# Performance work log

Hardware: AMD Instinct MI355X
Metric: run time of the kernel (lower is better)

## Reference

```python
import jax, jax.numpy as jnp
import numpy as np

B, S, D, H = 2, 2048, 64, 12  # batch, seq, richness (per-head dim), heads
NEG = -99999.0


def setup_inputs() -> dict:
    key = jax.random.key(0)
    ks = jax.random.split(key, 9)
    s_in = 1.0 / np.sqrt(D)
    s_out = 1.0 / np.sqrt(H * D)
    return {
        "x": jax.random.normal(ks[0], (B, S, D), dtype=jnp.float32),
        "Wq": jax.random.uniform(ks[1], (D, H * D), jnp.float32, -s_in, s_in),
        "bq": jax.random.uniform(ks[2], (H * D,), jnp.float32, -s_in, s_in),
        "Wk": jax.random.uniform(ks[3], (D, H * D), jnp.float32, -s_in, s_in),
        "bk": jax.random.uniform(ks[4], (H * D,), jnp.float32, -s_in, s_in),
        "Wv": jax.random.uniform(ks[5], (D, H * D), jnp.float32, -s_in, s_in),
        "bv": jax.random.uniform(ks[6], (H * D,), jnp.float32, -s_in, s_in),
        "Wo": jax.random.uniform(ks[7], (H * D, D), jnp.float32, -s_out, s_out),
        "bo": jax.random.uniform(ks[8], (D,), jnp.float32, -s_out, s_out),
    }


def reference(x, Wq, bq, Wk, bk, Wv, bv, Wo, bo):
    b, s, d = x.shape
    def split_heads(y):
        return y.reshape(b, s, H, d).transpose(0, 2, 1, 3)  # [B,H,S,D]
    q = split_heads(x @ Wq + bq)
    k = split_heads(x @ Wk + bk)
    v = split_heads(x @ Wv + bv)
    # NOTE: no 1/sqrt(d) scaling, faithful to original module.
    scores = jnp.einsum("bhqd,bhkd->bhqk", q, k)  # [B,H,S,S]
    # Faithful quirky mask: tril of the scores, then mask where it's zero.
    mask = jnp.tril(scores)
    scores = jnp.where(mask == 0, NEG, scores)
    p = jax.nn.softmax(scores, axis=-1)
    o = jnp.einsum("bhqk,bhkd->bhqd", p, v)  # [B,H,S,D]
    o = o.transpose(0, 2, 1, 3).reshape(b, s, H * d)
    return o @ Wo + bo
```

## Files before the change

### kernel.cpp

```cpp
#include <hip/hip_runtime.h>
#include <math.h>
#include <type_traits>

#define BB 2
#define SS 2048
#define DD 64
#define HH 12
#define C2FIX 23.083120654223414f

typedef _Float16 v8h __attribute__((ext_vector_type(8)));
typedef short    v8s __attribute__((ext_vector_type(8)));
typedef float    v4f __attribute__((ext_vector_type(4)));
typedef unsigned int v2u __attribute__((ext_vector_type(2)));

__device__ __forceinline__ unsigned short f2bf(float f) {
    unsigned u = __float_as_uint(f);
    u += 0x7FFF + ((u >> 16) & 1);
    return (unsigned short)(u >> 16);
}

__device__ __forceinline__ void async16(const void* g, void* l) {
    __builtin_amdgcn_global_load_lds(
        (const __attribute__((address_space(1))) unsigned int*)g,
        (__attribute__((address_space(3))) unsigned int*)l, 16, 0, 0);
}

__global__ __launch_bounds__(256) void prep_kernel(
    const float* __restrict__ x,
    const float* __restrict__ Wq, const float* __restrict__ Wk,
    const float* __restrict__ Wv, const float* __restrict__ Wo,
    _Float16* __restrict__ x16, _Float16* __restrict__ W16,
    _Float16* __restrict__ WoT)
{
    const int idx = blockIdx.x * 256 + threadIdx.x;
    if (idx < 262144) {
        x16[idx] = (_Float16)x[idx];
    } else if (idx < 262144 + 147456) {
        const int t = idx - 262144;
        const int k = t / 2304, c = t % 2304;
        const int mat = c / 768, cc = c % 768;
        const float* W = (mat == 0) ? Wq : (mat == 1) ? Wk : Wv;
        W16[c * 64 + k] = (_Float16)W[k * 768 + cc];
    } else {
        const int e = idx - 262144 - 147456;
        WoT[(e & 63) * 768 + (e >> 6)] = (_Float16)Wo[e];
    }
}

__global__ __launch_bounds__(256) void qkv_kernel(
    const _Float16* __restrict__ x16, const _Float16* __restrict__ W16,
    const float* __restrict__ bq, const float* __restrict__ bk,
    const float* __restrict__ bv,
    _Float16* __restrict__ Q16, _Float16* __restrict__ K16,
    unsigned short* __restrict__ VT)
{
    const int r0  = blockIdx.x * 64;
    const int c0g = blockIdx.y * 64;
    const int mat = c0g / 768, cc0 = c0g % 768;
    const int h   = cc0 >> 6;
    const int b   = r0 >> 11, s0 = r0 & 2047;

    const int wave = threadIdx.x >> 6, lane = threadIdx.x & 63;
    const int llow = lane & 15, quad = lane >> 4;
    const int rowbase = r0 + 16 * wave;

    const float* bias = (mat == 0) ? bq : (mat == 1) ? bk : bv;

    v8h a0 = *(const v8h*)(x16 + (size_t)(rowbase + llow) * 64 + quad * 8);
    v8h a1 = *(const v8h*)(x16 + (size_t)(rowbase + llow) * 64 + 32 + quad * 8);

    v4f acc[4];
    float bv4[4];
#pragma unroll
    for (int nb = 0; nb < 4; nb++) {
        const int col = c0g + 16 * nb + llow;
        v8h b0 = *(const v8h*)(W16 + (size_t)col * 64 + quad * 8);
        v8h b1 = *(const v8h*)(W16 + (size_t)col * 64 + 32 + quad * 8);
        v4f a = (v4f){0.f, 0.f, 0.f, 0.f};
        a = __builtin_amdgcn_mfma_f32_16x16x32_f16(a0, b0, a, 0, 0, 0);
        a = __builtin_amdgcn_mfma_f32_16x16x32_f16(a1, b1, a, 0, 0, 0);
        acc[nb] = a;
        bv4[nb] = bias[cc0 + 16 * nb + llow];
    }

    const int bh = b * HH + h;
    if (mat == 0) {
#pragma unroll
        for (int nb = 0; nb < 4; nb++)
#pragma unroll
            for (int r = 0; r < 4; r++) {
                const int s = s0 + 16 * wave + quad * 4 + r;
                Q16[((size_t)bh * SS + s) * 64 + 16 * nb + llow] =
                    (_Float16)((acc[nb][r] + bv4[nb]) * 1.4426950408889634f);
            }
    } else if (mat == 1) {
#pragma unroll
        for (int nb = 0; nb < 4; nb++)
#pragma unroll
            for (int r = 0; r < 4; r++) {
                const int s = s0 + 16 * wave + quad * 4 + r;
                K16[((size_t)bh * SS + s) * 64 + 16 * nb + llow] =
                    (_Float16)(acc[nb][r] + bv4[nb]);
            }
    } else {
#pragma unroll
        for (int nb = 0; nb < 4; nb++) {
            const int d = 16 * nb + llow;
            const int s = s0 + 16 * wave + quad * 4;
            unsigned short p0 = f2bf(acc[nb][0] + bv4[nb]);
            unsigned short p1 = f2bf(acc[nb][1] + bv4[nb]);
            unsigned short p2 = f2bf(acc[nb][2] + bv4[nb]);
            unsigned short p3 = f2bf(acc[nb][3] + bv4[nb]);
            v2u pk = (v2u){(unsigned)p0 | ((unsigned)p1 << 16),
                           (unsigned)p2 | ((unsigned)p3 << 16)};
            *(v2u*)&VT[((size_t)bh * 64 + d) * SS + s] = pk;
        }
    }
}

__global__ __launch_bounds__(256, 4) void attn_kernel(
    const _Float16* __restrict__ Q16, const _Float16* __restrict__ K16,
    const unsigned short* __restrict__ VTg, _Float16* __restrict__ O16)
{
    __shared__ __align__(16) _Float16       Kl[2][64 * 64];
    __shared__ __align__(16) unsigned short Vl[2][64 * 64];
    __shared__ __align__(16) unsigned short Pl[4][16 * 64];

    const int bh    = blockIdx.y;
    const int qtile = (int)((blockIdx.x + 11 * blockIdx.y) & 31);
    const int qBase = qtile * 64;
    const int wave  = threadIdx.x >> 6;
    const int lane  = threadIdx.x & 63;
    const int llow  = lane & 15;
    const int quad  = lane >> 4;
    const int q0    = qBase + 16 * wave;

    const _Float16*       Kp = K16 + (size_t)bh * SS * 64;
    const unsigned short* Vp = VTg + (size_t)bh * 64 * SS;

    const _Float16* Qp = Q16 + ((size_t)bh * SS + q0) * 64;
    v8h qa0 = *(const v8h*)(Qp + llow * 64 + quad * 8);
    v8h qa1 = *(const v8h*)(Qp + llow * 64 + 32 + quad * 8);

    v4f o[4];
    v4f ls = (v4f){0.f, 0.f, 0.f, 0.f};
    const short one_bf = (short)0x3F80;
    const v8s vones = (v8s){one_bf, one_bf, one_bf, one_bf,
                            one_bf, one_bf, one_bf, one_bf};
#pragma unroll
    for (int nb = 0; nb < 4; nb++) o[nb] = (v4f){0.f, 0.f, 0.f, 0.f};

    const int nt = qtile + 1;
    const int qrow = q0 + llow;
    const int sw = llow & 7;

#pragma unroll
    for (int rep = 0; rep < 2; rep++) {
        int c = rep * 256 + threadIdx.x;
        int row = c >> 3, g = (c & 7) ^ (row & 7);
        async16(Kp + (size_t)row * 64 + g * 8, &Kl[0][(rep * 256 + wave * 64) * 8]);
        async16(Vp + (size_t)row * SS + g * 8, &Vl[0][(rep * 256 + wave * 64) * 8]);
    }

    auto tile_body = [&](int t, auto masked_c) {
        constexpr bool MASKED = decltype(masked_c)::value;
        __syncthreads();
        if (t + 1 < nt) {
            const int ktn = (t + 1) * 64, bufn = (t + 1) & 1;
#pragma unroll
            for (int rep = 0; rep < 2; rep++) {
                int c = rep * 256 + threadIdx.x;
                int row = c >> 3, g = (c & 7) ^ (row & 7);
                async16(Kp + (size_t)(ktn + row) * 64 + g * 8,
                        &Kl[bufn][(rep * 256 + wave * 64) * 8]);
                async16(Vp + (size_t)row * SS + ktn + g * 8,
                        &Vl[bufn][(rep * 256 + wave * 64) * 8]);
            }
        }
        const int buf = t & 1, kt = t * 64;

        v4f sc[4];
#pragma unroll
        for (int cb = 0; cb < 4; cb++) {
            const int rk = 16 * cb + llow;
            v8h k0 = *(const v8h*)&Kl[buf][rk * 64 + ((quad ^ sw)) * 8];
            v8h k1 = *(const v8h*)&Kl[buf][rk * 64 + (((4 + quad) ^ sw)) * 8];
            v4f a2 = (v4f){0.f, 0.f, 0.f, 0.f};
            a2 = __builtin_amdgcn_mfma_f32_16x16x32_f16(k0, qa0, a2, 0, 0, 0);
            a2 = __builtin_amdgcn_mfma_f32_16x16x32_f16(k1, qa1, a2, 0, 0, 0);
            sc[cb] = a2;
        }

#pragma unroll
        for (int cb = 0; cb < 4; cb++) {
            const int kbase = kt + 16 * cb + quad * 4;
            unsigned dw[2];
#pragma unroll
            for (int h2 = 0; h2 < 2; h2++) {
                float pv2[2];
#pragma unroll
                for (int j2 = 0; j2 < 2; j2++) {
                    const int r = h2 * 2 + j2;
                    const float sv = sc[cb][r];
                    const float e  = __builtin_amdgcn_exp2f(sv - C2FIX);
                    float p;
                    if constexpr (MASKED)
                        p = (kbase + r <= qrow && sv != 0.f) ? e : 0.f;
                    else
                        p = (sv != 0.f) ? e : 0.f;
                    pv2[j2] = p;
                }
                dw[h2] = __builtin_amdgcn_perm(__float_as_uint(pv2[1]),
                                               __float_as_uint(pv2[0]),
                                               0x07060302u);
            }
            *(v2u*)&Pl[wave][llow * 64 + (((2 * cb + (quad >> 1)) ^ sw) * 8)
                             + (quad & 1) * 4] = (v2u){dw[0], dw[1]};
        }

        v8s pa0 = *(const v8s*)&Pl[wave][llow * 64 + ((quad ^ sw) * 8)];
        v8s pa1 = *(const v8s*)&Pl[wave][llow * 64 + (((4 + quad) ^ sw) * 8)];

        ls = __builtin_amdgcn_mfma_f32_16x16x32_bf16(pa0, vones, ls, 0, 0, 0);
        ls = __builtin_amdgcn_mfma_f32_16x16x32_bf16(pa1, vones, ls, 0, 0, 0);

#pragma unroll
        for (int nb = 0; nb < 4; nb++) {
            const int rv = 16 * nb + llow;
            v8s vv0 = *(const v8s*)&Vl[buf][rv * 64 + ((quad ^ sw)) * 8];
            v8s vv1 = *(const v8s*)&Vl[buf][rv * 64 + (((4 + quad) ^ sw)) * 8];
            o[nb] = __builtin_amdgcn_mfma_f32_16x16x32_bf16(pa0, vv0, o[nb], 0, 0, 0);
            o[nb] = __builtin_amdgcn_mfma_f32_16x16x32_bf16(pa1, vv1, o[nb], 0, 0, 0);
        }
    };

    for (int t = 0; t < nt - 1; t++) tile_body(t, std::false_type{});
    tile_body(nt - 1, std::true_type{});

    float ir[4];
#pragma unroll
    for (int r = 0; r < 4; r++)
        ir[r] = 1.0f / ls[r];
    _Float16* Op = O16 + ((size_t)bh * SS + q0) * 64;
#pragma unroll
    for (int nb = 0; nb < 4; nb++)
#pragma unroll
        for (int r = 0; r < 4; r++)
            Op[(quad * 4 + r) * 64 + 16 * nb + llow] = (_Float16)(o[nb][r] * ir[r]);
}

__global__ __launch_bounds__(256) void out_kernel(
    const _Float16* __restrict__ O16, const _Float16* __restrict__ WoT,
    const float* __restrict__ bo, float* __restrict__ out)
{
    __shared__ __align__(16) float red[4][16][66];
    const int r0   = blockIdx.x * 16;
    const int wave = threadIdx.x >> 6, lane = threadIdx.x & 63;
    const int llow = lane & 15, quad = lane >> 4;
    const int b = r0 >> 11, s = r0 & 2047;

    v4f acc[4];
#pragma unroll
    for (int cb = 0; cb < 4; cb++) acc[cb] = (v4f){0.f, 0.f, 0.f, 0.f};

#pragma unroll
    for (int i = 0; i < 6; i++) {
        const int kb = wave * 6 + i;
        const int h = kb >> 1, dseg = (kb & 1) * 32;
        v8h af = *(const v8h*)(O16 + ((size_t)(b * HH + h) * SS + s + llow) * 64 + dseg + quad * 8);
#pragma unroll
        for (int cb = 0; cb < 4; cb++) {
            v8h bf = *(const v8h*)(WoT + (size_t)(16 * cb + llow) * 768 + kb * 32 + quad * 8);
            acc[cb] = __builtin_amdgcn_mfma_f32_16x16x32_f16(af, bf, acc[cb], 0, 0, 0);
        }
    }

#pragma unroll
    for (int cb = 0; cb < 4; cb++)
#pragma unroll
        for (int r = 0; r < 4; r++)
            red[wave][quad * 4 + r][16 * cb + llow] = acc[cb][r];
    __syncthreads();

    const int col = threadIdx.x & 63, rr = threadIdx.x >> 6;
    const float bias = bo[col];
    for (int i = rr; i < 16; i += 4) {
        float sum = red[0][i][col] + red[1][i][col] + red[2][i][col] + red[3][i][col] + bias;
        out[(size_t)(r0 + i) * 64 + col] = sum;
    }
}

extern "C" void kernel_launch(void* const* d_in, const int* in_sizes, int n_in,
                              void* d_out, int out_size, void* d_ws, size_t ws_size,
                              hipStream_t stream)
{
    const float* x  = (const float*)d_in[0];
    const float* Wq = (const float*)d_in[1];
    const float* bq = (const float*)d_in[2];
    const float* Wk = (const float*)d_in[3];
    const float* bk = (const float*)d_in[4];
    const float* Wv = (const float*)d_in[5];
    const float* bv = (const float*)d_in[6];
    const float* Wo = (const float*)d_in[7];
    const float* bo = (const float*)d_in[8];
    float* out = (float*)d_out;

    char* w = (char*)d_ws;
    const size_t MB = 1024 * 1024;
    _Float16*       x16 = (_Float16*)(w);
    _Float16*       W16 = (_Float16*)(w + 512 * 1024);
    _Float16*       WoT = (_Float16*)(w + 832 * 1024);
    _Float16*       Q16 = (_Float16*)(w + 1 * MB);
    _Float16*       K16 = (_Float16*)(w + 7 * MB);
    unsigned short* VT  = (unsigned short*)(w + 13 * MB);
    _Float16*       O16 = (_Float16*)(w + 19 * MB);

    prep_kernel<<<1792, 256, 0, stream>>>(x, Wq, Wk, Wv, Wo, x16, W16, WoT);
    qkv_kernel<<<dim3(64, 36), 256, 0, stream>>>(x16, W16, bq, bk, bv, Q16, K16, VT);
    attn_kernel<<<dim3(32, BB * HH), 256, 0, stream>>>(Q16, K16, VT, O16);
    out_kernel<<<(BB * SS) / 16, 256, 0, stream>>>(O16, WoT, bo, out);
}
```

Baseline: 131.2 us.

## Split key tiles across two wave groups per attention block and reduce

Doubles the attention block to 512 threads, arranged as two 4-wave groups. Each group handles alternating key tiles for the same 64 query rows, with its own double-buffered K/V shared-memory staging. At the end, group 1 writes its partial output and row-sum accumulators to shared memory, and group 0 adds them and normalises. Because the softmax uses a fixed max offset, the partials combine by plain addition. The aim is to halve the serial key-loop length for long causal tiles and raise wave-level parallelism, at the cost of more LDS per block, an extra reduction step and idle waves in odd rounds.

```diff
diff --git a/kernel.cpp b/kernel.cpp
--- a/kernel.cpp
+++ b/kernel.cpp
@@ -118,22 +118,26 @@
     }
 }
 
-__global__ __launch_bounds__(256, 4) void attn_kernel(
+__global__ __launch_bounds__(512, 4) void attn_kernel(
     const _Float16* __restrict__ Q16, const _Float16* __restrict__ K16,
     const unsigned short* __restrict__ VTg, _Float16* __restrict__ O16)
 {
-    __shared__ __align__(16) _Float16       Kl[2][64 * 64];
-    __shared__ __align__(16) unsigned short Vl[2][64 * 64];
-    __shared__ __align__(16) unsigned short Pl[4][16 * 64];
+    __shared__ __align__(16) _Float16       Kl[2][2][64 * 64];
+    __shared__ __align__(16) unsigned short Vl[2][2][64 * 64];
+    __shared__ __align__(16) unsigned short Pl[8][16 * 64];
 
     const int bh    = blockIdx.y;
     const int qtile = (int)((blockIdx.x + 11 * blockIdx.y) & 31);
     const int qBase = qtile * 64;
     const int wave  = threadIdx.x >> 6;
+    const int grp   = wave >> 2;
+    const int gw    = wave & 3;
+    const int gtid  = threadIdx.x & 255;
     const int lane  = threadIdx.x & 63;
     const int llow  = lane & 15;
     const int quad  = lane >> 4;
-    const int q0    = qBase + 16 * wave;
+    const int q0    = qBase + 16 * gw;
+    const int sw    = llow & 7;
 
     const _Float16*       Kp = K16 + (size_t)bh * SS * 64;
     const unsigned short* Vp = VTg + (size_t)bh * 64 * SS;
@@ -151,40 +155,41 @@
     for (int nb = 0; nb < 4; nb++) o[nb] = (v4f){0.f, 0.f, 0.f, 0.f};
 
     const int nt = qtile + 1;
+    const int R  = (nt + 1) >> 1;
     const int qrow = q0 + llow;
-    const int sw = llow & 7;
-
-#pragma unroll
-    for (int rep = 0; rep < 2; rep++) {
-        int c = rep * 256 + threadIdx.x;
-        int row = c >> 3, g = (c & 7) ^ (row & 7);
-        async16(Kp + (size_t)row * 64 + g * 8, &Kl[0][(rep * 256 + wave * 64) * 8]);
-        async16(Vp + (size_t)row * SS + g * 8, &Vl[0][(rep * 256 + wave * 64) * 8]);
-    }
-
-    auto tile_body = [&](int t, auto masked_c) {
+
+    auto stage = [&](int kt, int b) {
+#pragma unroll
+        for (int rep = 0; rep < 2; rep++) {
+            int c = rep * 256 + gtid;
+            int row = c >> 3, g = (c & 7) ^ (row & 7);
+            async16(Kp + (size_t)(kt + row) * 64 + g * 8,
+                    &Kl[grp][b][(rep * 256 + gw * 64) * 8]);
+            async16(Vp + (size_t)row * SS + kt + g * 8,
+                    &Vl[grp][b][(rep * 256 + gw * 64) * 8]);
+        }
+    };
+
+    if (grp == 0)      stage(0, 0);
+    else if (nt > 1)   stage(64, 0);
+
+    auto round_body = [&](int r, auto masked_c) {
         constexpr bool MASKED = decltype(masked_c)::value;
         __syncthreads();
-        if (t + 1 < nt) {
-            const int ktn = (t + 1) * 64, bufn = (t + 1) & 1;
-#pragma unroll
-            for (int rep = 0; rep < 2; rep++) {
-                int c = rep * 256 + threadIdx.x;
-                int row = c >> 3, g = (c & 7) ^ (row & 7);
-                async16(Kp + (size_t)(ktn + row) * 64 + g * 8,
-                        &Kl[bufn][(rep * 256 + wave * 64) * 8]);
-                async16(Vp + (size_t)row * SS + ktn + g * 8,
-                        &Vl[bufn][(rep * 256 + wave * 64) * 8]);
-            }
-        }
-        const int buf = t & 1, kt = t * 64;
+        {
+            const int tn = 2 * (r + 1) + grp;
+            if (tn < nt) stage(tn * 64, (r + 1) & 1);
+        }
+        const int t = 2 * r + grp;
+        if (t >= nt) return;
+        const int buf = r & 1, kt = t * 64;
 
         v4f sc[4];
 #pragma unroll
         for (int cb = 0; cb < 4; cb++) {
             const int rk = 16 * cb + llow;
-            v8h k0 = *(const v8h*)&Kl[buf][rk * 64 + ((quad ^ sw)) * 8];
-            v8h k1 = *(const v8h*)&Kl[buf][rk * 64 + (((4 + quad) ^ sw)) * 8];
+            v8h k0 = *(const v8h*)&Kl[grp][buf][rk * 64 + ((quad ^ sw)) * 8];
+            v8h k1 = *(const v8h*)&Kl[grp][buf][rk * 64 + (((4 + quad) ^ sw)) * 8];
             v4f a2 = (v4f){0.f, 0.f, 0.f, 0.f};
             a2 = __builtin_amdgcn_mfma_f32_16x16x32_f16(k0, qa0, a2, 0, 0, 0);
             a2 = __builtin_amdgcn_mfma_f32_16x16x32_f16(k1, qa1, a2, 0, 0, 0);
@@ -200,12 +205,12 @@
                 float pv2[2];
 #pragma unroll
                 for (int j2 = 0; j2 < 2; j2++) {
-                    const int r = h2 * 2 + j2;
-                    const float sv = sc[cb][r];
+                    const int rr = h2 * 2 + j2;
+                    const float sv = sc[cb][rr];
                     const float e  = __builtin_amdgcn_exp2f(sv - C2FIX);
                     float p;
                     if constexpr (MASKED)
-                        p = (kbase + r <= qrow && sv != 0.f) ? e : 0.f;
+                        p = (kbase + rr <= qrow && sv != 0.f) ? e : 0.f;
                     else
                         p = (sv != 0.f) ? e : 0.f;
                     pv2[j2] = p;
@@ -227,26 +232,45 @@
 #pragma unroll
         for (int nb = 0; nb < 4; nb++) {
             const int rv = 16 * nb + llow;
-            v8s vv0 = *(const v8s*)&Vl[buf][rv * 64 + ((quad ^ sw)) * 8];
-            v8s vv1 = *(const v8s*)&Vl[buf][rv * 64 + (((4 + quad) ^ sw)) * 8];
+            v8s vv0 = *(const v8s*)&Vl[grp][buf][rv * 64 + ((quad ^ sw)) * 8];
+            v8s vv1 = *(const v8s*)&Vl[grp][buf][rv * 64 + (((4 + quad) ^ sw)) * 8];
             o[nb] = __builtin_amdgcn_mfma_f32_16x16x32_bf16(pa0, vv0, o[nb], 0, 0, 0);
             o[nb] = __builtin_amdgcn_mfma_f32_16x16x32_bf16(pa1, vv1, o[nb], 0, 0, 0);
         }
     };
 
-    for (int t = 0; t < nt - 1; t++) tile_body(t, std::false_type{});
-    tile_body(nt - 1, std::true_type{});
-
-    float ir[4];
-#pragma unroll
-    for (int r = 0; r < 4; r++)
-        ir[r] = 1.0f / ls[r];
-    _Float16* Op = O16 + ((size_t)bh * SS + q0) * 64;
-#pragma unroll
-    for (int nb = 0; nb < 4; nb++)
+    for (int r = 0; r < R - 1; r++) round_body(r, std::false_type{});
+    round_body(R - 1, std::true_type{});
+
+    __syncthreads();
+
+    float* oShare  = (float*)&Kl[1][0][0];
+    float* lsShare = (float*)&Vl[1][0][0];
+    if (grp == 1) {
+        const int sl = (gw * 64 + lane) * 4;
+#pragma unroll
+        for (int nb = 0; nb < 4; nb++)
+            *(v4f*)&oShare[nb * 1024 + sl] = o[nb];
+        *(v4f*)&lsShare[sl] = ls;
+    }
+    __syncthreads();
+    if (grp == 0) {
+        const int sl = (gw * 64 + lane) * 4;
+#pragma unroll
+        for (int nb = 0; nb < 4; nb++)
+            o[nb] += *(const v4f*)&oShare[nb * 1024 + sl];
+        ls += *(const v4f*)&lsShare[sl];
+        float ir[4];
 #pragma unroll
         for (int r = 0; r < 4; r++)
-            Op[(quad * 4 + r) * 64 + 16 * nb + llow] = (_Float16)(o[nb][r] * ir[r]);
+            ir[r] = 1.0f / ls[r];
+        _Float16* Op = O16 + ((size_t)bh * SS + q0) * 64;
+#pragma unroll
+        for (int nb = 0; nb < 4; nb++)
+#pragma unroll
+            for (int r = 0; r < 4; r++)
+                Op[(quad * 4 + r) * 64 + 16 * nb + llow] = (_Float16)(o[nb][r] * ir[r]);
+    }
 }
 
 __global__ __launch_bounds__(256) void out_kernel(
@@ -317,6 +341,6 @@
 
     prep_kernel<<<1792, 256, 0, stream>>>(x, Wq, Wk, Wv, Wo, x16, W16, WoT);
     qkv_kernel<<<dim3(64, 36), 256, 0, stream>>>(x16, W16, bq, bk, bv, Q16, K16, VT);
-    attn_kernel<<<dim3(32, BB * HH), 256, 0, stream>>>(Q16, K16, VT, O16);
+    attn_kernel<<<dim3(32, BB * HH), 512, 0, stream>>>(Q16, K16, VT, O16);
     out_kernel<<<(BB * SS) / 16, 256, 0, stream>>>(O16, WoT, bo, out);
 }
```

After: 136.5 us. 1.04x slower.

## Feed softmax probabilities to PV MFMA directly from registers, dropping LDS staging

Applied to the files above, without the earlier changes.

The P tile is no longer written to and reread from a per-wave LDS buffer. Instead the score accumulator layout is used directly as the A operand of 16x16x16 bf16 MFMAs, with V fragments read to match that layout. This removes LDS stores/loads and the implied wait for the P round trip, and frees shared memory. In exchange it issues twice as many smaller MFMAs, which have lower throughput per instruction than the 16x16x32 form, and uses more registers to hold V fragments.

```diff
diff --git a/kernel.cpp b/kernel.cpp
--- a/kernel.cpp
+++ b/kernel.cpp
@@ -10,6 +10,7 @@
 
 typedef _Float16 v8h __attribute__((ext_vector_type(8)));
 typedef short    v8s __attribute__((ext_vector_type(8)));
+typedef short    v4s __attribute__((ext_vector_type(4)));
 typedef float    v4f __attribute__((ext_vector_type(4)));
 typedef unsigned int v2u __attribute__((ext_vector_type(2)));
 
@@ -124,7 +125,6 @@
 {
     __shared__ __align__(16) _Float16       Kl[2][64 * 64];
     __shared__ __align__(16) unsigned short Vl[2][64 * 64];
-    __shared__ __align__(16) unsigned short Pl[4][16 * 64];
 
     const int bh    = blockIdx.y;
     const int qtile = (int)((blockIdx.x + 11 * blockIdx.y) & 31);
@@ -145,8 +145,7 @@
     v4f o[4];
     v4f ls = (v4f){0.f, 0.f, 0.f, 0.f};
     const short one_bf = (short)0x3F80;
-    const v8s vones = (v8s){one_bf, one_bf, one_bf, one_bf,
-                            one_bf, one_bf, one_bf, one_bf};
+    const v4s vones = (v4s){one_bf, one_bf, one_bf, one_bf};
 #pragma unroll
     for (int nb = 0; nb < 4; nb++) o[nb] = (v4f){0.f, 0.f, 0.f, 0.f};
 
@@ -191,6 +190,17 @@
             sc[cb] = a2;
         }
 
+        v4s vvf[4][4];
+#pragma unroll
+        for (int nb = 0; nb < 4; nb++) {
+            const int rv = 16 * nb + llow;
+#pragma unroll
+            for (int cb = 0; cb < 4; cb++)
+                vvf[nb][cb] = *(const v4s*)&Vl[buf][rv * 64 +
+                                (((2 * cb + (quad >> 1)) ^ sw) * 8) + (quad & 1) * 4];
+        }
+
+        v4s pA[4];
 #pragma unroll
         for (int cb = 0; cb < 4; cb++) {
             const int kbase = kt + 16 * cb + quad * 4;
@@ -214,24 +224,20 @@
                                                __float_as_uint(pv2[0]),
                                                0x07060302u);
             }
-            *(v2u*)&Pl[wave][llow * 64 + (((2 * cb + (quad >> 1)) ^ sw) * 8)
-                             + (quad & 1) * 4] = (v2u){dw[0], dw[1]};
-        }
-
-        v8s pa0 = *(const v8s*)&Pl[wave][llow * 64 + ((quad ^ sw) * 8)];
-        v8s pa1 = *(const v8s*)&Pl[wave][llow * 64 + (((4 + quad) ^ sw) * 8)];
-
-        ls = __builtin_amdgcn_mfma_f32_16x16x32_bf16(pa0, vones, ls, 0, 0, 0);
-        ls = __builtin_amdgcn_mfma_f32_16x16x32_bf16(pa1, vones, ls, 0, 0, 0);
-
-#pragma unroll
-        for (int nb = 0; nb < 4; nb++) {
-            const int rv = 16 * nb + llow;
-            v8s vv0 = *(const v8s*)&Vl[buf][rv * 64 + ((quad ^ sw)) * 8];
-            v8s vv1 = *(const v8s*)&Vl[buf][rv * 64 + (((4 + quad) ^ sw)) * 8];
-            o[nb] = __builtin_amdgcn_mfma_f32_16x16x32_bf16(pa0, vv0, o[nb], 0, 0, 0);
-            o[nb] = __builtin_amdgcn_mfma_f32_16x16x32_bf16(pa1, vv1, o[nb], 0, 0, 0);
-        }
+            v2u pk = (v2u){dw[0], dw[1]};
+            pA[cb] = *(const v4s*)&pk;
+        }
+
+#pragma unroll
+        for (int cb = 0; cb < 4; cb++)
+            ls = __builtin_amdgcn_mfma_f32_16x16x16bf16_1k(pA[cb], vones, ls, 0, 0, 0);
+
+#pragma unroll
+        for (int nb = 0; nb < 4; nb++)
+#pragma unroll
+            for (int cb = 0; cb < 4; cb++)
+                o[nb] = __builtin_amdgcn_mfma_f32_16x16x16bf16_1k(
+                            pA[cb], vvf[nb][cb], o[nb], 0, 0, 0);
     };
 
     for (int t = 0; t < nt - 1; t++) tile_body(t, std::false_type{});
```

New measurement: 135.7 us. +3.4%, slower.
